# Performance work log

Hardware: AMD Instinct MI355X
Metric: run time of the kernel (lower is better)

## Reference

```python
import jax, jax.numpy as jnp
import numpy as np

HIDDEN = 2048
HEADS = 16
KV_HEADS = 1
HEAD_DIM = 128
SEQ = 2048
BATCH = 1
LAM = 0.5


def _rotate_half(x):
    h = x.shape[-1] // 2
    return jnp.concatenate([-x[..., h:], x[..., :h]], axis=-1)


def _apply_rope(t, cos, sin):
    # t: [B,S,H,D], cos/sin: [S,D] -> broadcast over batch & heads
    c = cos[None, :, None, :]
    s = sin[None, :, None, :]
    return t * c + _rotate_half(t) * s


def setup_inputs() -> dict:
    key = jax.random.key(0)
    ks = jax.random.split(key, 8)
    x = jax.random.normal(ks[0], (BATCH, SEQ, HIDDEN), dtype=jnp.float32)
    # realistic RoPE tables, rotate-half layout: [S, D]
    inv_freq = 1.0 / (10000.0 ** (np.arange(0, HEAD_DIM, 2, dtype=np.float32) / HEAD_DIM))
    t = np.arange(SEQ, dtype=np.float32)
    ang = np.outer(t, inv_freq)                      # [S, D/2]
    ang = np.concatenate([ang, ang], axis=-1)        # [S, D]
    freqs_cos = jnp.asarray(np.cos(ang))
    freqs_sin = jnp.asarray(np.sin(ang))
    mask = jnp.tril(jnp.ones((SEQ, SEQ), dtype=bool))  # causal, True = attend
    scale = 1.0 / np.sqrt(HIDDEN)
    q1_w = jax.random.normal(ks[1], (HIDDEN, HEADS * HEAD_DIM), dtype=jnp.float32) * scale
    q2_w = jax.random.normal(ks[2], (HIDDEN, HEADS * HEAD_DIM), dtype=jnp.float32) * scale
    k_w = jax.random.normal(ks[3], (HIDDEN, KV_HEADS * HEAD_DIM), dtype=jnp.float32) * scale
    v_w = jax.random.normal(ks[4], (HIDDEN, KV_HEADS * HEAD_DIM), dtype=jnp.float32) * scale
    out_w = jax.random.normal(ks[5], (HEADS * HEAD_DIM, HIDDEN), dtype=jnp.float32) * scale
    return {"x": x, "freqs_cos": freqs_cos, "freqs_sin": freqs_sin, "mask": mask,
            "q1_w": q1_w, "q2_w": q2_w, "k_w": k_w, "v_w": v_w, "out_w": out_w}


def reference(x, freqs_cos, freqs_sin, mask, q1_w, q2_w, k_w, v_w, out_w):
    B, S, _ = x.shape
    q1 = (x @ q1_w).reshape(B, S, HEADS, HEAD_DIM)
    q2 = (x @ q2_w).reshape(B, S, HEADS, HEAD_DIM)
    k = (x @ k_w).reshape(B, S, KV_HEADS, HEAD_DIM)
    v = (x @ v_w).reshape(B, S, KV_HEADS, HEAD_DIM)
    q1 = _apply_rope(q1, freqs_cos, freqs_sin)
    q2 = _apply_rope(q2, freqs_cos, freqs_sin)
    k = _apply_rope(k, freqs_cos, freqs_sin)
    # MQA broadcast of the single KV head
    k = jnp.repeat(k, HEADS // KV_HEADS, axis=2)  # [B,S,H,D]
    v = jnp.repeat(v, HEADS // KV_HEADS, axis=2)
    inv_sqrt_d = 1.0 / jnp.sqrt(jnp.float32(HEAD_DIM))
    s1 = jnp.einsum('bqhd,bkhd->bhqk', q1, k) * inv_sqrt_d
    s2 = jnp.einsum('bqhd,bkhd->bhqk', q2, k) * inv_sqrt_d
    m = mask[None, None, :, :]
    neg = jnp.float32(-1e10)
    s1 = jnp.where(m, s1, neg)
    s2 = jnp.where(m, s2, neg)
    a1 = jax.nn.softmax(s1, axis=-1)
    a2 = jax.nn.softmax(s2, axis=-1)
    a = a1 - LAM * a2
    a = a / (jnp.sum(a, axis=-1, keepdims=True) + 1e-8)
    a = jnp.maximum(a, 0.0)
    out = jnp.einsum('bhqk,bkhd->bqhd', a, v).reshape(B, S, HEADS * HEAD_DIM)
    return out @ out_w
```

## Files before the change

kernel.cpp:

```cpp
#include <hip/hip_runtime.h>
#include <hip/hip_bf16.h>

typedef __attribute__((ext_vector_type(8))) short bf16x8;
typedef __attribute__((ext_vector_type(4))) float f32x4;

#define MFMA16(a, b, c) __builtin_amdgcn_mfma_f32_16x16x32_bf16((a), (b), (c), 0, 0, 0)

#define LDQ 4352
#define KSCALE 0.12751743f

__device__ __forceinline__ ushort f2bf(float f) {
    unsigned int x = __float_as_uint(f);
    x += 0x7fffu + ((x >> 16) & 1u);
    return (ushort)(x >> 16);
}
__device__ __forceinline__ float bf2f(ushort u) {
    return __uint_as_float(((unsigned int)u) << 16);
}
__device__ __forceinline__ float exp2_fast(float x) {
    float r;
    asm("v_exp_f32 %0, %1" : "=v"(r) : "v"(x));
    return r;
}
__device__ __forceinline__ unsigned int cvtpk(float lo, float hi) {
    unsigned int r;
    asm("v_cvt_pk_bf16_f32 %0, %1, %2" : "=v"(r) : "v"(lo), "v"(hi));
    return r;
}

__device__ __forceinline__ void gload16(const ushort* g, ushort* l) {
    __builtin_amdgcn_global_load_lds((const __attribute__((address_space(1))) unsigned int*)g,
                                     (__attribute__((address_space(3))) unsigned int*)l, 16, 0, 0);
}

__global__ __launch_bounds__(256) void prep_k(const float* __restrict__ x, ushort* __restrict__ xb,
                                              const float* __restrict__ q1w, const float* __restrict__ q2w,
                                              const float* __restrict__ kw, const float* __restrict__ vw,
                                              const float* __restrict__ ow,
                                              ushort* __restrict__ w1t, ushort* __restrict__ w2t,
                                              ushort* __restrict__ wkt, ushort* __restrict__ wvt,
                                              ushort* __restrict__ wot) {
    int bid = blockIdx.x;
    if (bid < 4096) {
        int i = bid * 256 + threadIdx.x;
        float4 v = ((const float4*)x)[i];
        ushort4 u;
        u.x = f2bf(v.x); u.y = f2bf(v.y); u.z = f2bf(v.z); u.w = f2bf(v.w);
        ((ushort4*)xb)[i] = u;
        return;
    }
    bid -= 4096;
    const float* in;
    ushort* out;
    int C, TX;
    if (bid < 4096) { in = q1w; out = w1t; C = 2048; TX = 64; }
    else if (bid < 8192) { bid -= 4096; in = q2w; out = w2t; C = 2048; TX = 64; }
    else if (bid < 12288) { bid -= 8192; in = ow; out = wot; C = 2048; TX = 64; }
    else if (bid < 12544) { bid -= 12288; in = kw; out = wkt; C = 128; TX = 4; }
    else { bid -= 12544; in = vw; out = wvt; C = 128; TX = 4; }
    __shared__ ushort t[32][33];
    const int c0 = (bid % TX) * 32, r0 = (bid / TX) * 32;
    const int lx = threadIdx.x & 31, ly = threadIdx.x >> 5;
#pragma unroll
    for (int i = 0; i < 4; ++i)
        t[ly + i * 8][lx] = f2bf(in[(size_t)(r0 + ly + i * 8) * C + c0 + lx]);
    __syncthreads();
#pragma unroll
    for (int i = 0; i < 4; ++i)
        out[(size_t)(c0 + ly + i * 8) * 2048 + r0 + lx] = t[lx][ly + i * 8];
}

template <bool FUSE>
__global__ __launch_bounds__(512) void gemm8_k(const ushort* __restrict__ A, int lda,
                                               const ushort* __restrict__ Bt, int ldb,
                                               void* __restrict__ C, int ldc,
                                               int K, int nbx, int cbf,
                                               const float* __restrict__ cs,
                                               const float* __restrict__ sn,
                                               ushort* __restrict__ vtb) {
    __shared__ ushort As[2 * 4096];
    __shared__ ushort Bs[2 * 4096];
    const int tid = threadIdx.x;
    const int lane = tid & 63, wid = tid >> 6;
    const int cpx = (int)gridDim.x >> 3;
    const int swz = ((int)blockIdx.x & 7) * cpx + ((int)blockIdx.x >> 3);
    const int nt = swz / nbx;
    const int m0 = (swz % nbx) * 128, n0 = nt * 128;
    const int wr = wid >> 2, wc = wid & 3;
    const int l15 = lane & 15, lhi = lane >> 4;

    const int srow = tid >> 2;
    const int scol = (((tid & 3) ^ ((srow >> 1) & 3)) << 3);
    const ushort* gA = A + (size_t)(m0 + srow) * lda + scol;
    const ushort* gB = Bt + (size_t)(n0 + srow) * ldb + scol;
    ushort* lA = &As[wid * 512];
    ushort* lB = &Bs[wid * 512];

    f32x4 acc[4][2];
#pragma unroll
    for (int m = 0; m < 4; ++m)
#pragma unroll
        for (int n = 0; n < 2; ++n) acc[m][n] = (f32x4){0.f, 0.f, 0.f, 0.f};

    const int fcol = (lhi << 4) ^ (((l15 >> 1) & 3) << 4);

    gload16(gA, lA);
    gload16(gB, lB);
    __syncthreads();

    int cur = 0;
    for (int k0 = 0; k0 < K; k0 += 32) {
        if (k0 + 32 < K) {
            gload16(gA + k0 + 32, lA + (cur ^ 1) * 4096);
            gload16(gB + k0 + 32, lB + (cur ^ 1) * 4096);
        }
        const char* aB = (const char*)&As[cur * 4096];
        const char* bB = (const char*)&Bs[cur * 4096];
        bf16x8 af[4], bfr[2];
#pragma unroll
        for (int m = 0; m < 4; ++m)
            af[m] = *(const bf16x8*)(aB + (wr * 64 + m * 16 + l15) * 64 + fcol);
#pragma unroll
        for (int n = 0; n < 2; ++n)
            bfr[n] = *(const bf16x8*)(bB + (wc * 16 + n * 64 + l15) * 64 + fcol);
#pragma unroll
        for (int m = 0; m < 4; ++m)
#pragma unroll
            for (int n = 0; n < 2; ++n)
                acc[m][n] = MFMA16(af[m], bfr[n], acc[m][n]);
        __syncthreads();
        cur ^= 1;
    }

    if (FUSE) {
        if (nt == 33) {
#pragma unroll
            for (int m = 0; m < 4; ++m) {
                const int rb = m0 + wr * 64 + m * 16 + lhi * 4;
#pragma unroll
                for (int n = 0; n < 2; ++n) {
                    const int d = wc * 16 + n * 64 + l15;
                    uint2 w;
                    w.x = cvtpk(acc[m][n][0], acc[m][n][1]);
                    w.y = cvtpk(acc[m][n][2], acc[m][n][3]);
                    *(uint2*)(vtb + (size_t)d * 2048 + rb) = w;
                }
            }
        } else {
            const float scale = (nt == 32) ? KSCALE : 1.0f;
            ushort* out = (ushort*)C;
            const int d0 = wc * 16 + l15;
#pragma unroll
            for (int m = 0; m < 4; ++m) {
                const int rb = m0 + wr * 64 + m * 16 + lhi * 4;
#pragma unroll
                for (int r = 0; r < 4; ++r) {
                    const int row = rb + r;
                    float c0 = cs[row * 128 + d0], c1 = cs[row * 128 + d0 + 64];
                    float s0 = sn[row * 128 + d0], s1 = sn[row * 128 + d0 + 64];
                    float t0 = acc[m][0][r], t1 = acc[m][1][r];
                    out[(size_t)row * ldc + n0 + d0] = f2bf((t0 * c0 - t1 * s0) * scale);
                    out[(size_t)row * ldc + n0 + d0 + 64] = f2bf((t1 * c1 + t0 * s1) * scale);
                }
            }
        }
    } else {
#pragma unroll
        for (int m = 0; m < 4; ++m) {
            const int rb = m0 + wr * 64 + m * 16 + lhi * 4;
#pragma unroll
            for (int n = 0; n < 2; ++n) {
                const int col = n0 + wc * 16 + n * 64 + l15;
#pragma unroll
                for (int r = 0; r < 4; ++r) {
                    if (cbf)
                        ((ushort*)C)[(size_t)(rb + r) * ldc + col] = f2bf(acc[m][n][r]);
                    else
                        ((float*)C)[(size_t)(rb + r) * ldc + col] = acc[m][n][r];
                }
            }
        }
    }
}


__device__ __forceinline__ void stage_k_chunk(const ushort* __restrict__ kb, int kc,
                                              ushort* __restrict__ kbuf, int wid, int lane) {
#pragma unroll
    for (int u = 0; u < 2; ++u) {
        const int w = wid * 2 + u;
        const int row = w * 4 + (lane >> 4);
        const int colb = ((lane & 15) * 16) ^ ((row & 7) << 4);
        gload16(kb + (size_t)(kc + row) * LDQ + (colb >> 1), kbuf + w * 512);
    }
}

__device__ __forceinline__ void stage_v_chunk(const ushort* __restrict__ vtb, int kc,
                                              ushort* __restrict__ vbuf, int wid, int lane) {
#pragma unroll
    for (int u = 0; u < 2; ++u) {
        const int w = wid * 2 + u;
        const int rowd = w * 16 + (lane >> 2);
        const int colb = ((lane & 3) * 16) ^ (((rowd >> 1) & 3) << 4);
        gload16(vtb + (size_t)rowd * 2048 + kc + (colb >> 1), vbuf + w * 512);
    }
}

__device__ __forceinline__ void load_k_frags(const ushort* __restrict__ kbuf, int l15, int lhi,
                                             bf16x8 kf[2][4]) {
    const char* kB = (const char*)kbuf;
#pragma unroll
    for (int n2 = 0; n2 < 2; ++n2) {
        const int r = n2 * 16 + l15;
#pragma unroll
        for (int c = 0; c < 4; ++c)
            kf[n2][c] = *(const bf16x8*)(kB + r * 256 + ((lhi * 16 + c * 64) ^ ((r & 7) << 4)));
    }
}

template <bool MASKED>
__device__ __forceinline__ void sums_chunk(const ushort* __restrict__ kbuf, int kc,
                                           int l15, int lhi, int qrow,
                                           const bf16x8* q1f, const bf16x8* q2f,
                                           float& sum1, float& sum2) {
    bf16x8 kf[2][4];
    load_k_frags(kbuf, l15, lhi, kf);
    f32x4 s1[2], s2[2];
#pragma unroll
    for (int n2 = 0; n2 < 2; ++n2) {
        s1[n2] = (f32x4){0.f, 0.f, 0.f, 0.f};
        s2[n2] = (f32x4){0.f, 0.f, 0.f, 0.f};
#pragma unroll
        for (int c = 0; c < 4; ++c) {
            s1[n2] = MFMA16(kf[n2][c], q1f[c], s1[n2]);
            s2[n2] = MFMA16(kf[n2][c], q2f[c], s2[n2]);
        }
    }
    const int kbase = kc + lhi * 4;
#pragma unroll
    for (int n2 = 0; n2 < 2; ++n2)
#pragma unroll
        for (int r = 0; r < 4; ++r) {
            float e1 = exp2_fast(s1[n2][r]);
            float e2 = exp2_fast(s2[n2][r]);
            if (MASKED) {
                bool ok = (kbase + n2 * 16 + r) <= qrow;
                e1 = ok ? e1 : 0.f;
                e2 = ok ? e2 : 0.f;
            }
            sum1 += e1;
            sum2 += e2;
        }
}

__global__ __launch_bounds__(256) void attn_sums_k(const ushort* __restrict__ qkv,
                                                   float* __restrict__ sums) {
    __shared__ ushort Kbuf[2 * 4096];
    const int bid = blockIdx.x;
    const int strip = 127 - (bid >> 3);
    const int cs = (bid >> 2) & 1;
    const int hg = bid & 3;
    const int q0 = strip << 4;
    const int lane = threadIdx.x & 63, wid = threadIdx.x >> 6;
    const int h = hg * 4 + wid;
    const int l15 = lane & 15, lhi = lane >> 4;
    const int qrow = q0 + l15;
    const ushort* kb = qkv + 4096;

    bf16x8 q1f[4], q2f[4];
    {
        size_t base = (size_t)qrow * LDQ + h * 128 + lhi * 8;
#pragma unroll
        for (int c = 0; c < 4; ++c) {
            q1f[c] = *(const bf16x8*)(qkv + base + c * 32);
            q2f[c] = *(const bf16x8*)(qkv + base + 2048 + c * 32);
        }
    }

    const int nchunk = (strip >> 1) + 1;
    const int ndiag = nchunk - 1;
    const int nch = (nchunk - cs + 1) >> 1;

    float sum1 = 0.f, sum2 = 0.f;
    if (nch > 0) stage_k_chunk(kb, cs * 32, Kbuf, wid, lane);
    __syncthreads();
    for (int i = 0; i < nch; ++i) {
        const int ch = cs + 2 * i, kc = ch << 5;
        if (i + 1 < nch) stage_k_chunk(kb, kc + 64, Kbuf + ((i + 1) & 1) * 4096, wid, lane);
        const ushort* kcur = Kbuf + (i & 1) * 4096;
        if (ch == ndiag)
            sums_chunk<true>(kcur, kc, l15, lhi, qrow, q1f, q2f, sum1, sum2);
        else
            sums_chunk<false>(kcur, kc, l15, lhi, qrow, q1f, q2f, sum1, sum2);
        __syncthreads();
    }

    sum1 += __shfl_xor(sum1, 16);
    sum1 += __shfl_xor(sum1, 32);
    sum2 += __shfl_xor(sum2, 16);
    sum2 += __shfl_xor(sum2, 32);

    if (lhi == 0) {
        sums[(size_t)((cs * 2 + 0) * 16 + h) * 2048 + qrow] = sum1;
        sums[(size_t)((cs * 2 + 1) * 16 + h) * 2048 + qrow] = sum2;
    }
}

template <bool MASKED>
__device__ __forceinline__ void pv_chunk(const ushort* __restrict__ kbuf, const ushort* __restrict__ vbuf,
                                         int kc, ushort* __restrict__ Pb,
                                         int l15, int lhi, int qrow,
                                         const bf16x8* q1f, const bf16x8* q2f,
                                         float c1, float c2, f32x4* o) {
    bf16x8 kf[2][4];
    load_k_frags(kbuf, l15, lhi, kf);
    bf16x8 vf[8];
    const char* vB = (const char*)vbuf;
#pragma unroll
    for (int dt = 0; dt < 8; ++dt) {
        const int d = dt * 16 + l15;
        vf[dt] = *(const bf16x8*)(vB + d * 64 + ((lhi * 16) ^ (((d >> 1) & 3) << 4)));
    }
    f32x4 s1[2], s2[2];
#pragma unroll
    for (int n2 = 0; n2 < 2; ++n2) {
        s1[n2] = (f32x4){0.f, 0.f, 0.f, 0.f};
        s2[n2] = (f32x4){0.f, 0.f, 0.f, 0.f};
#pragma unroll
        for (int c = 0; c < 4; ++c) {
            s1[n2] = MFMA16(kf[n2][c], q1f[c], s1[n2]);
            s2[n2] = MFMA16(kf[n2][c], q2f[c], s2[n2]);
        }
    }
    const int kbase = kc + lhi * 4;
#pragma unroll
    for (int n2 = 0; n2 < 2; ++n2) {
        float p[4];
#pragma unroll
        for (int r = 0; r < 4; ++r) {
            float e1 = exp2_fast(s1[n2][r]) * c1;
            float e2 = exp2_fast(s2[n2][r]) * c2;
            float pv = fmaxf(e1 - e2, 0.f);
            if (MASKED) pv = ((kbase + n2 * 16 + r) <= qrow) ? pv : 0.f;
            p[r] = pv;
        }
        uint2 w;
        w.x = cvtpk(p[0], p[1]);
        w.y = cvtpk(p[2], p[3]);
        *(uint2*)(Pb + l15 * 40 + n2 * 16 + lhi * 4) = w;
    }
    asm volatile("s_waitcnt lgkmcnt(0)" ::: "memory");
    bf16x8 pf = *(const bf16x8*)(Pb + l15 * 40 + lhi * 8);
#pragma unroll
    for (int dt = 0; dt < 8; ++dt)
        o[dt] = MFMA16(pf, vf[dt], o[dt]);
}

__global__ __launch_bounds__(256) void attn_pv_k(const ushort* __restrict__ qkv,
                                                 const ushort* __restrict__ vtb,
                                                 const float* __restrict__ sums,
                                                 ushort* __restrict__ op0,
                                                 ushort* __restrict__ op1) {
    __shared__ ushort Kbuf[2 * 4096];
    __shared__ ushort Vbuf[2 * 4096];
    __shared__ ushort P[4][16][40];
    const int bid = blockIdx.x;
    const int strip = 127 - (bid >> 3);
    const int cs = (bid >> 2) & 1;
    const int hg = bid & 3;
    const int q0 = strip << 4;
    const int lane = threadIdx.x & 63, wid = threadIdx.x >> 6;
    const int h = hg * 4 + wid;
    const int l15 = lane & 15, lhi = lane >> 4;
    const int qrow = q0 + l15;
    const ushort* kb = qkv + 4096;

    bf16x8 q1f[4], q2f[4];
    {
        size_t base = (size_t)qrow * LDQ + h * 128 + lhi * 8;
#pragma unroll
        for (int c = 0; c < 4; ++c) {
            q1f[c] = *(const bf16x8*)(qkv + base + c * 32);
            q2f[c] = *(const bf16x8*)(qkv + base + 2048 + c * 32);
        }
    }

    const float sum1 = sums[(size_t)(0 * 16 + h) * 2048 + qrow] + sums[(size_t)(2 * 16 + h) * 2048 + qrow];
    const float sum2 = sums[(size_t)(1 * 16 + h) * 2048 + qrow] + sums[(size_t)(3 * 16 + h) * 2048 + qrow];
    const float inv_denom = 1.0f / (0.5f + 1e-8f);
    const float c1 = inv_denom / sum1;
    const float c2 = 0.5f * inv_denom / sum2;

    f32x4 o[8];
#pragma unroll
    for (int dt = 0; dt < 8; ++dt) o[dt] = (f32x4){0.f, 0.f, 0.f, 0.f};

    const int nchunk = (strip >> 1) + 1;
    const int ndiag = nchunk - 1;
    const int nch = (nchunk - cs + 1) >> 1;

    if (nch > 0) {
        stage_k_chunk(kb, cs * 32, Kbuf, wid, lane);
        stage_v_chunk(vtb, cs * 32, Vbuf, wid, lane);
    }
    __syncthreads();
    for (int i = 0; i < nch; ++i) {
        const int ch = cs + 2 * i, kc = ch << 5;
        if (i + 1 < nch) {
            stage_k_chunk(kb, kc + 64, Kbuf + ((i + 1) & 1) * 4096, wid, lane);
            stage_v_chunk(vtb, kc + 64, Vbuf + ((i + 1) & 1) * 4096, wid, lane);
        }
        const ushort* kcur = Kbuf + (i & 1) * 4096;
        const ushort* vcur = Vbuf + (i & 1) * 4096;
        ushort* Pb = &P[wid][0][0];
        if (ch == ndiag)
            pv_chunk<true>(kcur, vcur, kc, Pb, l15, lhi, qrow, q1f, q2f, c1, c2, o);
        else
            pv_chunk<false>(kcur, vcur, kc, Pb, l15, lhi, qrow, q1f, q2f, c1, c2, o);
        __syncthreads();
    }

    ushort* op = cs ? op1 : op0;
#pragma unroll
    for (int dt = 0; dt < 8; ++dt)
#pragma unroll
        for (int r = 0; r < 4; ++r)
            op[(size_t)(q0 + lhi * 4 + r) * 2048 + h * 128 + dt * 16 + l15] = f2bf(o[dt][r]);
}

__device__ __forceinline__ unsigned int addbf2(unsigned int a, unsigned int b) {
    float alo = bf2f((ushort)a), ahi = bf2f((ushort)(a >> 16));
    float blo = bf2f((ushort)b), bhi = bf2f((ushort)(b >> 16));
    return (unsigned int)f2bf(alo + blo) | ((unsigned int)f2bf(ahi + bhi) << 16);
}
__global__ void combine_k(const ushort* __restrict__ o0, const ushort* __restrict__ o1,
                          ushort* __restrict__ out, int n8) {
    int i = blockIdx.x * blockDim.x + threadIdx.x;
    if (i >= n8) return;
    uint4 a = ((const uint4*)o0)[i];
    uint4 b = ((const uint4*)o1)[i];
    uint4 c;
    c.x = addbf2(a.x, b.x);
    c.y = addbf2(a.y, b.y);
    c.z = addbf2(a.z, b.z);
    c.w = addbf2(a.w, b.w);
    ((uint4*)out)[i] = c;
}

extern "C" void kernel_launch(void* const* d_in, const int* in_sizes, int n_in,
                              void* d_out, int out_size, void* d_ws, size_t ws_size,
                              hipStream_t stream) {
    const int S = 2048, HID = 2048;

    const float* x = (const float*)d_in[0];
    const float* fcos = (const float*)d_in[1];
    const float* fsin = (const float*)d_in[2];
    const float* q1w = (const float*)d_in[4];
    const float* q2w = (const float*)d_in[5];
    const float* kw = (const float*)d_in[6];
    const float* vw = (const float*)d_in[7];
    const float* ow = (const float*)d_in[8];

    ushort* xb = (ushort*)d_ws;
    ushort* btq = xb + (size_t)4194304;
    ushort* w1t = btq;
    ushort* w2t = btq + (size_t)2048 * 2048;
    ushort* wkt = btq + (size_t)4096 * 2048;
    ushort* wvt = btq + (size_t)4224 * 2048;
    ushort* wot = btq + (size_t)8912896;
    ushort* qkvb = wot + (size_t)4194304;
    ushort* vtb = qkvb + (size_t)8912896;
    float* sums = (float*)(vtb + (size_t)262144);
    ushort* opart0 = xb;
    ushort* opart1 = w1t;
    ushort* aob = w2t;

    prep_k<<<dim3(16896), dim3(256), 0, stream>>>(x, xb, q1w, q2w, kw, vw, ow,
                                                  w1t, w2t, wkt, wvt, wot);

    gemm8_k<true><<<dim3(544), dim3(512), 0, stream>>>(xb, HID, btq, HID, qkvb, LDQ, HID, 16, 1,
                                                       fcos, fsin, vtb);

    attn_sums_k<<<dim3(1024), dim3(256), 0, stream>>>(qkvb, sums);

    attn_pv_k<<<dim3(1024), dim3(256), 0, stream>>>(qkvb, vtb, sums, opart0, opart1);

    combine_k<<<dim3(2048), dim3(256), 0, stream>>>(opart0, opart1, aob, S * HID / 8);

    gemm8_k<false><<<dim3(256), dim3(512), 0, stream>>>(aob, HID, wot, HID, (float*)d_out, HID, HID, 16, 0,
                                                        nullptr, nullptr, nullptr);
}
```

Measured before the change: 179.3 us.

## Deepen GEMM LDS pipeline to four stages with partial vmcnt waits

The GEMM kernel moves from a double-buffered LDS scheme to a four-slot ring with three tiles in flight. It waits with explicit partial vmcnt counts and raw s_barrier instead of __syncthreads, and raises wave priority around the MFMA block. The attention sums and PV loops also swap full syncs for partial vmcnt waits, so the next chunk's global loads can stay outstanding while the current one is computed. This costs double the LDS in the GEMM, which may lower occupancy, and it relies on the vmcnt counts matching how many loads gload16 and the stage functions actually issue.

Result: slower. 209.1 us (+16.6%).

```diff
diff --git a/kernel.cpp b/kernel.cpp
--- a/kernel.cpp
+++ b/kernel.cpp
@@ -78,8 +78,8 @@
                                                const float* __restrict__ cs,
                                                const float* __restrict__ sn,
                                                ushort* __restrict__ vtb) {
-    __shared__ ushort As[2 * 4096];
-    __shared__ ushort Bs[2 * 4096];
+    __shared__ ushort As[4 * 4096];
+    __shared__ ushort Bs[4 * 4096];
     const int tid = threadIdx.x;
     const int lane = tid & 63, wid = tid >> 6;
     const int cpx = (int)gridDim.x >> 3;
@@ -104,18 +104,9 @@
 
     const int fcol = (lhi << 4) ^ (((l15 >> 1) & 3) << 4);
 
-    gload16(gA, lA);
-    gload16(gB, lB);
-    __syncthreads();
-
-    int cur = 0;
-    for (int k0 = 0; k0 < K; k0 += 32) {
-        if (k0 + 32 < K) {
-            gload16(gA + k0 + 32, lA + (cur ^ 1) * 4096);
-            gload16(gB + k0 + 32, lB + (cur ^ 1) * 4096);
-        }
-        const char* aB = (const char*)&As[cur * 4096];
-        const char* bB = (const char*)&Bs[cur * 4096];
+    auto compute = [&](int i) {
+        const char* aB = (const char*)&As[(i & 3) * 4096];
+        const char* bB = (const char*)&Bs[(i & 3) * 4096];
         bf16x8 af[4], bfr[2];
 #pragma unroll
         for (int m = 0; m < 4; ++m)
@@ -123,14 +114,43 @@
 #pragma unroll
         for (int n = 0; n < 2; ++n)
             bfr[n] = *(const bf16x8*)(bB + (wc * 16 + n * 64 + l15) * 64 + fcol);
+        __builtin_amdgcn_s_setprio(1);
 #pragma unroll
         for (int m = 0; m < 4; ++m)
 #pragma unroll
             for (int n = 0; n < 2; ++n)
                 acc[m][n] = MFMA16(af[m], bfr[n], acc[m][n]);
-        __syncthreads();
-        cur ^= 1;
-    }
+        __builtin_amdgcn_s_setprio(0);
+    };
+
+    const int NS = K >> 5;
+#pragma unroll
+    for (int s = 0; s < 3; ++s) {
+        gload16(gA + s * 32, lA + s * 4096);
+        gload16(gB + s * 32, lB + s * 4096);
+    }
+    int i = 0;
+    for (; i < NS - 3; ++i) {
+        gload16(gA + (i + 3) * 32, lA + ((i + 3) & 3) * 4096);
+        gload16(gB + (i + 3) * 32, lB + ((i + 3) & 3) * 4096);
+        asm volatile("s_waitcnt vmcnt(6)" ::: "memory");
+        __builtin_amdgcn_s_barrier();
+        compute(i);
+        __builtin_amdgcn_s_barrier();
+    }
+    asm volatile("s_waitcnt vmcnt(4)" ::: "memory");
+    __builtin_amdgcn_s_barrier();
+    compute(i);
+    __builtin_amdgcn_s_barrier();
+    ++i;
+    asm volatile("s_waitcnt vmcnt(2)" ::: "memory");
+    __builtin_amdgcn_s_barrier();
+    compute(i);
+    __builtin_amdgcn_s_barrier();
+    ++i;
+    asm volatile("s_waitcnt vmcnt(0)" ::: "memory");
+    __builtin_amdgcn_s_barrier();
+    compute(i);
 
     if (FUSE) {
         if (nt == 33) {
@@ -283,16 +303,21 @@
 
     float sum1 = 0.f, sum2 = 0.f;
     if (nch > 0) stage_k_chunk(kb, cs * 32, Kbuf, wid, lane);
-    __syncthreads();
     for (int i = 0; i < nch; ++i) {
         const int ch = cs + 2 * i, kc = ch << 5;
-        if (i + 1 < nch) stage_k_chunk(kb, kc + 64, Kbuf + ((i + 1) & 1) * 4096, wid, lane);
+        if (i + 1 < nch) {
+            stage_k_chunk(kb, kc + 64, Kbuf + ((i + 1) & 1) * 4096, wid, lane);
+            asm volatile("s_waitcnt vmcnt(2)" ::: "memory");
+        } else {
+            asm volatile("s_waitcnt vmcnt(0)" ::: "memory");
+        }
+        __builtin_amdgcn_s_barrier();
         const ushort* kcur = Kbuf + (i & 1) * 4096;
         if (ch == ndiag)
             sums_chunk<true>(kcur, kc, l15, lhi, qrow, q1f, q2f, sum1, sum2);
         else
             sums_chunk<false>(kcur, kc, l15, lhi, qrow, q1f, q2f, sum1, sum2);
-        __syncthreads();
+        __builtin_amdgcn_s_barrier();
     }
 
     sum1 += __shfl_xor(sum1, 16);
@@ -403,13 +428,16 @@
         stage_k_chunk(kb, cs * 32, Kbuf, wid, lane);
         stage_v_chunk(vtb, cs * 32, Vbuf, wid, lane);
     }
-    __syncthreads();
     for (int i = 0; i < nch; ++i) {
         const int ch = cs + 2 * i, kc = ch << 5;
         if (i + 1 < nch) {
             stage_k_chunk(kb, kc + 64, Kbuf + ((i + 1) & 1) * 4096, wid, lane);
             stage_v_chunk(vtb, kc + 64, Vbuf + ((i + 1) & 1) * 4096, wid, lane);
-        }
+            asm volatile("s_waitcnt vmcnt(4)" ::: "memory");
+        } else {
+            asm volatile("s_waitcnt vmcnt(0)" ::: "memory");
+        }
+        __builtin_amdgcn_s_barrier();
         const ushort* kcur = Kbuf + (i & 1) * 4096;
         const ushort* vcur = Vbuf + (i & 1) * 4096;
         ushort* Pb = &P[wid][0][0];
@@ -417,7 +445,7 @@
             pv_chunk<true>(kcur, vcur, kc, Pb, l15, lhi, qrow, q1f, q2f, c1, c2, o);
         else
             pv_chunk<false>(kcur, vcur, kc, Pb, l15, lhi, qrow, q1f, q2f, c1, c2, o);
-        __syncthreads();
+        __builtin_amdgcn_s_barrier();
     }
 
     ushort* op = cs ? op1 : op0;
```

## Split-K the output projection and relax attention loop barriers

Applied to the files above, without the earlier changes.

The output GEMM is split into two K-slices. This doubles the grid to 512 blocks so more CUs are busy, and each slice writes bf16 partials that a new opadd kernel sums into fp32. Separately, the attention sums and PV loops replace __syncthreads with explicit vmcnt waits plus raw s_barrier, so the next chunk's prefetch can stay in flight while the current chunk is computed. The cost is an extra kernel launch, extra memory traffic for the partials, and bf16 rounding of the partials before the final add.

New measurement: 181.0 us. Within noise of the previous version (+0.9%).

```diff
diff --git a/kernel.cpp b/kernel.cpp
--- a/kernel.cpp
+++ b/kernel.cpp
@@ -74,7 +74,8 @@
 __global__ __launch_bounds__(512) void gemm8_k(const ushort* __restrict__ A, int lda,
                                                const ushort* __restrict__ Bt, int ldb,
                                                void* __restrict__ C, int ldc,
-                                               int K, int nbx, int cbf,
+                                               int K, int nbx, int ntile, int cbf,
+                                               size_t cstride,
                                                const float* __restrict__ cs,
                                                const float* __restrict__ sn,
                                                ushort* __restrict__ vtb) {
@@ -84,13 +85,15 @@
     const int lane = tid & 63, wid = tid >> 6;
     const int cpx = (int)gridDim.x >> 3;
     const int swz = ((int)blockIdx.x & 7) * cpx + ((int)blockIdx.x >> 3);
-    const int nt = swz / nbx;
-    const int m0 = (swz % nbx) * 128, n0 = nt * 128;
+    const int kslice = swz / ntile;
+    const int tile = swz - kslice * ntile;
+    const int nt = tile / nbx;
+    const int m0 = (tile - nt * nbx) * 128, n0 = nt * 128;
     const int wr = wid >> 2, wc = wid & 3;
     const int l15 = lane & 15, lhi = lane >> 4;
 
     const int srow = tid >> 2;
-    const int scol = (((tid & 3) ^ ((srow >> 1) & 3)) << 3);
+    const int scol = (((tid & 3) ^ ((srow >> 1) & 3)) << 3) + kslice * K;
     const ushort* gA = A + (size_t)(m0 + srow) * lda + scol;
     const ushort* gB = Bt + (size_t)(n0 + srow) * ldb + scol;
     ushort* lA = &As[wid * 512];
@@ -165,6 +168,7 @@
             }
         }
     } else {
+        char* Cp = (char*)C + kslice * cstride;
 #pragma unroll
         for (int m = 0; m < 4; ++m) {
             const int rb = m0 + wr * 64 + m * 16 + lhi * 4;
@@ -174,9 +178,9 @@
 #pragma unroll
                 for (int r = 0; r < 4; ++r) {
                     if (cbf)
-                        ((ushort*)C)[(size_t)(rb + r) * ldc + col] = f2bf(acc[m][n][r]);
+                        ((ushort*)Cp)[(size_t)(rb + r) * ldc + col] = f2bf(acc[m][n][r]);
                     else
-                        ((float*)C)[(size_t)(rb + r) * ldc + col] = acc[m][n][r];
+                        ((float*)Cp)[(size_t)(rb + r) * ldc + col] = acc[m][n][r];
                 }
             }
         }
@@ -283,16 +287,21 @@
 
     float sum1 = 0.f, sum2 = 0.f;
     if (nch > 0) stage_k_chunk(kb, cs * 32, Kbuf, wid, lane);
-    __syncthreads();
     for (int i = 0; i < nch; ++i) {
         const int ch = cs + 2 * i, kc = ch << 5;
-        if (i + 1 < nch) stage_k_chunk(kb, kc + 64, Kbuf + ((i + 1) & 1) * 4096, wid, lane);
+        if (i + 1 < nch) {
+            stage_k_chunk(kb, kc + 64, Kbuf + ((i + 1) & 1) * 4096, wid, lane);
+            asm volatile("s_waitcnt vmcnt(2)" ::: "memory");
+        } else {
+            asm volatile("s_waitcnt vmcnt(0)" ::: "memory");
+        }
+        __builtin_amdgcn_s_barrier();
         const ushort* kcur = Kbuf + (i & 1) * 4096;
         if (ch == ndiag)
             sums_chunk<true>(kcur, kc, l15, lhi, qrow, q1f, q2f, sum1, sum2);
         else
             sums_chunk<false>(kcur, kc, l15, lhi, qrow, q1f, q2f, sum1, sum2);
-        __syncthreads();
+        __builtin_amdgcn_s_barrier();
     }
 
     sum1 += __shfl_xor(sum1, 16);
@@ -403,13 +412,16 @@
         stage_k_chunk(kb, cs * 32, Kbuf, wid, lane);
         stage_v_chunk(vtb, cs * 32, Vbuf, wid, lane);
     }
-    __syncthreads();
     for (int i = 0; i < nch; ++i) {
         const int ch = cs + 2 * i, kc = ch << 5;
         if (i + 1 < nch) {
             stage_k_chunk(kb, kc + 64, Kbuf + ((i + 1) & 1) * 4096, wid, lane);
             stage_v_chunk(vtb, kc + 64, Vbuf + ((i + 1) & 1) * 4096, wid, lane);
-        }
+            asm volatile("s_waitcnt vmcnt(4)" ::: "memory");
+        } else {
+            asm volatile("s_waitcnt vmcnt(0)" ::: "memory");
+        }
+        __builtin_amdgcn_s_barrier();
         const ushort* kcur = Kbuf + (i & 1) * 4096;
         const ushort* vcur = Vbuf + (i & 1) * 4096;
         ushort* Pb = &P[wid][0][0];
@@ -417,7 +429,7 @@
             pv_chunk<true>(kcur, vcur, kc, Pb, l15, lhi, qrow, q1f, q2f, c1, c2, o);
         else
             pv_chunk<false>(kcur, vcur, kc, Pb, l15, lhi, qrow, q1f, q2f, c1, c2, o);
-        __syncthreads();
+        __builtin_amdgcn_s_barrier();
     }
 
     ushort* op = cs ? op1 : op0;
@@ -445,6 +457,25 @@
     c.z = addbf2(a.z, b.z);
     c.w = addbf2(a.w, b.w);
     ((uint4*)out)[i] = c;
+}
+
+__global__ void opadd_k(const ushort* __restrict__ p0, const ushort* __restrict__ p1,
+                        float* __restrict__ out, int n8) {
+    int i = blockIdx.x * blockDim.x + threadIdx.x;
+    if (i >= n8) return;
+    uint4 a = ((const uint4*)p0)[i];
+    uint4 b = ((const uint4*)p1)[i];
+    float4 r0, r1;
+    r0.x = bf2f((ushort)a.x) + bf2f((ushort)b.x);
+    r0.y = bf2f((ushort)(a.x >> 16)) + bf2f((ushort)(b.x >> 16));
+    r0.z = bf2f((ushort)a.y) + bf2f((ushort)b.y);
+    r0.w = bf2f((ushort)(a.y >> 16)) + bf2f((ushort)(b.y >> 16));
+    r1.x = bf2f((ushort)a.z) + bf2f((ushort)b.z);
+    r1.y = bf2f((ushort)(a.z >> 16)) + bf2f((ushort)(b.z >> 16));
+    r1.z = bf2f((ushort)a.w) + bf2f((ushort)b.w);
+    r1.w = bf2f((ushort)(a.w >> 16)) + bf2f((ushort)(b.w >> 16));
+    ((float4*)out)[i * 2] = r0;
+    ((float4*)out)[i * 2 + 1] = r1;
 }
 
 extern "C" void kernel_launch(void* const* d_in, const int* in_sizes, int n_in,
@@ -478,8 +509,8 @@
     prep_k<<<dim3(16896), dim3(256), 0, stream>>>(x, xb, q1w, q2w, kw, vw, ow,
                                                   w1t, w2t, wkt, wvt, wot);
 
-    gemm8_k<true><<<dim3(544), dim3(512), 0, stream>>>(xb, HID, btq, HID, qkvb, LDQ, HID, 16, 1,
-                                                       fcos, fsin, vtb);
+    gemm8_k<true><<<dim3(544), dim3(512), 0, stream>>>(xb, HID, btq, HID, qkvb, LDQ, HID, 16, 544, 1,
+                                                       0, fcos, fsin, vtb);
 
     attn_sums_k<<<dim3(1024), dim3(256), 0, stream>>>(qkvb, sums);
 
@@ -487,6 +518,8 @@
 
     combine_k<<<dim3(2048), dim3(256), 0, stream>>>(opart0, opart1, aob, S * HID / 8);
 
-    gemm8_k<false><<<dim3(256), dim3(512), 0, stream>>>(aob, HID, wot, HID, (float*)d_out, HID, HID, 16, 0,
-                                                        nullptr, nullptr, nullptr);
-}
+    gemm8_k<false><<<dim3(512), dim3(512), 0, stream>>>(aob, HID, wot, HID, xb, HID, 1024, 16, 256, 1,
+                                                        (size_t)4194304 * 2, nullptr, nullptr, nullptr);
+
+    opadd_k<<<dim3(2048), dim3(256), 0, stream>>>(xb, w1t, (float*)d_out, S * HID / 8);
+}
```
